# Performance work log

Hardware: AMD Instinct MI355X
Metric: run time of the kernel (lower is better)

Reference implementation:

```python
import jax, jax.numpy as jnp
import numpy as np

B, S, D, H = 2, 2048, 1024, 16
HD = D // H
MAX_SEQ_LEN = 2048
ROPE_BASE = 10000.0


def _rope(x, pos):
    # x: [B,S,H,HD], pos: [B,S] int positions (already abs+clamped)
    inv_freq = 1.0 / (ROPE_BASE ** (jnp.arange(0, HD, 2, dtype=jnp.float32) / HD))  # [HD/2]
    freqs = pos.astype(jnp.float32)[..., None] * inv_freq  # [B,S,HD/2]
    cos = jnp.cos(freqs)[:, :, None, :]  # [B,S,1,HD/2]
    sin = jnp.sin(freqs)[:, :, None, :]
    x1, x2 = x[..., : HD // 2], x[..., HD // 2 :]
    return jnp.concatenate([x1 * cos - x2 * sin, x2 * cos + x1 * sin], axis=-1)


def setup_inputs() -> dict:
    key = jax.random.key(0)
    ks = jax.random.split(key, 8)
    std = 1.0 / np.sqrt(D)
    x = jax.random.normal(ks[0], (B, S, D), dtype=jnp.float32)
    Wq = jax.random.normal(ks[1], (D, D), dtype=jnp.float32) * std
    Wk = jax.random.normal(ks[2], (D, D), dtype=jnp.float32) * std
    Wv = jax.random.normal(ks[3], (D, D), dtype=jnp.float32) * std
    Wo = jax.random.normal(ks[4], (D, D), dtype=jnp.float32) * std
    bq = jnp.zeros((D,), jnp.float32)
    bk = jnp.zeros((D,), jnp.float32)
    bv = jnp.zeros((D,), jnp.float32)
    bo = jnp.zeros((D,), jnp.float32)
    decay_rate = jnp.float32(0.1)
    # causal mask [B,S,S]
    mask = jnp.broadcast_to(jnp.tril(jnp.ones((S, S), jnp.int32)), (B, S, S))
    # sorted day offsets per batch (monotone time axis)
    days_offset = jnp.sort(jax.random.randint(ks[5], (B, S), 0, MAX_SEQ_LEN), axis=-1).astype(jnp.int32)
    return {"x": x, "Wq": Wq, "bq": bq, "Wk": Wk, "bk": bk, "Wv": Wv, "bv": bv,
            "Wo": Wo, "bo": bo, "decay_rate": decay_rate, "mask": mask, "days_offset": days_offset}


def reference(x, Wq, bq, Wk, bk, Wv, bv, Wo, bo, decay_rate, mask, days_offset):
    b, s, _ = x.shape
    q = (x @ Wq.T + bq).reshape(b, s, H, HD)
    k = (x @ Wk.T + bk).reshape(b, s, H, HD)
    v = (x @ Wv.T + bv).reshape(b, s, H, HD)
    pos = jnp.clip(jnp.abs(days_offset), 0, MAX_SEQ_LEN - 1)
    q = _rope(q, pos)
    k = _rope(k, pos)
    scores = jnp.einsum("bqhd,bkhd->bhqk", q, k) / np.sqrt(HD).astype(np.float32)
    dist = jnp.abs(days_offset[:, :, None] - days_offset[:, None, :]).astype(jnp.float32)  # [B,S,S]
    decay = jnp.exp(-decay_rate * dist)
    scores = scores * decay[:, None, :, :]
    scores = jnp.where(mask[:, None, :, :] == 0, -jnp.inf, scores)
    attn = jax.nn.softmax(scores, axis=-1)
    out = jnp.einsum("bhqk,bkhd->bqhd", attn, v).reshape(b, s, D)
    return out @ Wo.T + bo
```

## Files before the change

### kernel.cpp

```cpp
#include <hip/hip_runtime.h>
#include <hip/hip_bf16.h>


typedef unsigned short u16;
typedef short bf16x8 __attribute__((ext_vector_type(8)));
typedef float f32x4 __attribute__((ext_vector_type(4)));

__device__ __forceinline__ u16 f2bf(float f) {
    unsigned u = __builtin_bit_cast(unsigned, f);
    u += 0x7fffu + ((u >> 16) & 1u);
    return (u16)(u >> 16);
}
__device__ __forceinline__ float bf2f(u16 h) {
    unsigned u = ((unsigned)h) << 16;
    return __builtin_bit_cast(float, u);
}

__global__ __launch_bounds__(256) void convert_all_k(const float* __restrict__ x,
                                                     const float* __restrict__ wq,
                                                     const float* __restrict__ wk,
                                                     const float* __restrict__ wv,
                                                     const float* __restrict__ wo_,
                                                     u16* __restrict__ xb,
                                                     u16* __restrict__ wqkv,
                                                     u16* __restrict__ wob) {
    int i = (blockIdx.x * 256 + threadIdx.x) * 4;
    const float* src;
    u16* dst;
    int off;
    if (i < 4194304) {
        src = x; dst = xb; off = i;
    } else if (i < 5242880) {
        src = wq; dst = wqkv; off = i - 4194304;
    } else if (i < 6291456) {
        src = wk; dst = wqkv + 1048576; off = i - 5242880;
    } else if (i < 7340032) {
        src = wv; dst = wqkv + 2097152; off = i - 6291456;
    } else {
        src = wo_; dst = wob; off = i - 7340032;
    }
    float4 v = *(const float4*)(src + off);
    uint2 o;
    o.x = (unsigned)f2bf(v.x) | ((unsigned)f2bf(v.y) << 16);
    o.y = (unsigned)f2bf(v.z) | ((unsigned)f2bf(v.w) << 16);
    *(uint2*)(dst + off) = o;
}

template <int EPI>
__global__ __launch_bounds__(256) void gemm_bt(const u16* __restrict__ A,
                                               const u16* __restrict__ Bw,
                                               const float* __restrict__ bias0,
                                               const float* __restrict__ bias1,
                                               const float* __restrict__ bias2,
                                               const int* __restrict__ days,
                                               u16* __restrict__ outB,
                                               float* __restrict__ outF,
                                               int M, int N, int K) {
    __shared__ __align__(16) u16 As[2][4096];
    __shared__ __align__(16) u16 Bs[2][4096];
    const int tid = threadIdx.x;
    const int lane = tid & 63;
    const int w = tid >> 6;
    const int wr = w >> 1, wc = w & 1;
    const int lr = lane & 15, lg = lane >> 4;
    const int nbn = N >> 7;
    const int m0 = (blockIdx.x / nbn) << 7;
    const int n0 = (blockIdx.x % nbn) << 7;

    f32x4 acc[4][4] = {};

    const u16* aptr[2];
    const u16* bptr[2];
    int ldsoff[2];
#pragma unroll
    for (int i = 0; i < 2; ++i) {
        int c = (w * 2 + i) * 64 + lane;
        int row = c >> 2, kc = (c & 3) << 3;
        aptr[i] = A + (size_t)(m0 + row) * K + kc;
        bptr[i] = Bw + (size_t)(n0 + row) * K + kc;
        ldsoff[i] = (w * 2 + i) * 512;
    }

#define GSTAGE(K0, BUF)                                                                \
    do {                                                                               \
        _Pragma("unroll") for (int i = 0; i < 2; ++i) {                                \
            __builtin_amdgcn_global_load_lds(                                          \
                (const __attribute__((address_space(1))) void*)(aptr[i] + (K0)),       \
                (__attribute__((address_space(3))) void*)(&As[BUF][ldsoff[i]]), 16, 0, \
                0);                                                                    \
            __builtin_amdgcn_global_load_lds(                                          \
                (const __attribute__((address_space(1))) void*)(bptr[i] + (K0)),       \
                (__attribute__((address_space(3))) void*)(&Bs[BUF][ldsoff[i]]), 16, 0, \
                0);                                                                    \
        }                                                                              \
    } while (0)

    const int nks = K >> 5;
    GSTAGE(0, 0);
    for (int ks = 0; ks < nks; ++ks) {
        const int cur = ks & 1;
        if (ks + 1 < nks) {
            GSTAGE((ks + 1) * 32, cur ^ 1);
            asm volatile("s_waitcnt vmcnt(4)" ::: "memory");
        } else {
            asm volatile("s_waitcnt vmcnt(0)" ::: "memory");
        }
        __builtin_amdgcn_s_barrier();
        bf16x8 af[4], bfr[4];
#pragma unroll
        for (int i = 0; i < 4; ++i)
            af[i] = *(const bf16x8*)(&As[cur][(wr * 64 + i * 16 + lr) * 32 + lg * 8]);
#pragma unroll
        for (int j = 0; j < 4; ++j)
            bfr[j] = *(const bf16x8*)(&Bs[cur][(wc * 64 + j * 16 + lr) * 32 + lg * 8]);
#pragma unroll
        for (int i = 0; i < 4; ++i)
#pragma unroll
            for (int j = 0; j < 4; ++j)
                acc[i][j] = __builtin_amdgcn_mfma_f32_16x16x32_bf16(af[i], bfr[j],
                                                                    acc[i][j], 0, 0, 0);
        __builtin_amdgcn_s_barrier();
    }
#undef GSTAGE

    auto bsel = [&](int ng) -> float {
        if (EPI != 0) return bias0[ng];
        return (ng < 1024) ? bias0[ng] : (ng < 2048) ? bias1[ng - 1024] : bias2[ng - 2048];
    };

    if (EPI == 0 && (n0 + wc * 64) < 2048) {
        const float C1 = -0.41524101186091903f;
        const float inv0 = exp2f((float)lr * C1);
        const float inv1 = exp2f((float)(16 + lr) * C1);
#pragma unroll
        for (int i = 0; i < 4; ++i) {
            int mg = m0 + wr * 64 + i * 16 + lg * 4;
#pragma unroll
            for (int r = 0; r < 4; ++r) {
                int m = mg + r;
                int d = days[m];
                int ad = d < 0 ? -d : d;
                ad = ad > 2047 ? 2047 : ad;
                float pos = (float)ad;
#pragma unroll
                for (int j = 0; j < 2; ++j) {
                    int ng1 = n0 + wc * 64 + j * 16 + lr;
                    int ng2 = ng1 + 32;
                    float x1 = acc[i][j][r] + bsel(ng1);
                    float x2 = acc[i][j + 2][r] + bsel(ng2);
                    float ang = pos * (j ? inv1 : inv0);
                    float sn, cs;
                    __sincosf(ang, &sn, &cs);
                    outB[(size_t)m * N + ng1] = f2bf(x1 * cs - x2 * sn);
                    outB[(size_t)m * N + ng2] = f2bf(x2 * cs + x1 * sn);
                }
            }
        }
    } else {
#pragma unroll
        for (int i = 0; i < 4; ++i) {
            int mg = m0 + wr * 64 + i * 16 + lg * 4;
#pragma unroll
            for (int j = 0; j < 4; ++j) {
                int ng = n0 + wc * 64 + j * 16 + lr;
                float bias = bsel(ng);
#pragma unroll
                for (int r = 0; r < 4; ++r) {
                    float v = acc[i][j][r] + bias;
                    if (EPI == 0)
                        outB[(size_t)(mg + r) * N + ng] = f2bf(v);
                    else
                        outF[(size_t)(mg + r) * N + ng] = v;
                }
            }
        }
    }
}

__global__ __launch_bounds__(256) void v_transpose_k(const u16* __restrict__ qkv,
                                                     u16* __restrict__ vt) {
    __shared__ u16 tile[64][66];
    int st = blockIdx.x & 31;
    int bh = blockIdx.x >> 5;
    int b = bh >> 4, h = bh & 15;
    int s0 = st * 64;
    int t = threadIdx.x;
#pragma unroll
    for (int it = 0; it < 16; ++it) {
        int idx = it * 256 + t;
        int sr = idx >> 6, c = idx & 63;
        tile[sr][c] = qkv[(size_t)(b * 2048 + s0 + sr) * 3072 + 2048 + h * 64 + c];
    }
    __syncthreads();
#pragma unroll
    for (int it = 0; it < 16; ++it) {
        int idx = it * 256 + t;
        int hd = idx >> 6, sc = idx & 63;
        vt[((size_t)(bh * 64 + hd)) * 2048 + s0 + sc] = tile[sc][hd];
    }
}

__device__ __forceinline__ void attn_tile(const u16* __restrict__ Ks,
                                          const u16* __restrict__ Vs,
                                          u16* __restrict__ Pw,
                                          const int* __restrict__ dbk,
                                          float dkmax_c, bf16x8 pconst, float pcr,
                                          bf16x8 bq0, bf16x8 bq1, float dq_c, float c1,
                                          int qrel, bool domask,
                                          float& l_part, f32x4* acc, int lr, int lg) {
    if (!domask && __all(dkmax_c - dq_c < -20.0f)) {
        l_part += 16.0f * pcr;
        __builtin_amdgcn_s_setprio(1);
#pragma unroll
        for (int pv = 0; pv < 2; ++pv) {
            int chunk = pv * 4 + lg;
#pragma unroll
            for (int c = 0; c < 4; ++c) {
                const int r3 = c * 16 + lr;
                bf16x8 bv = *(const bf16x8*)(Vs + r3 * 64 + ((chunk ^ (r3 & 7)) << 3));
                acc[c] = __builtin_amdgcn_mfma_f32_16x16x32_bf16(pconst, bv, acc[c], 0, 0, 0);
            }
        }
        __builtin_amdgcn_s_setprio(0);
        return;
    }
    f32x4 st_acc[4];
    __builtin_amdgcn_s_setprio(1);
#pragma unroll
    for (int st = 0; st < 4; ++st) {
        const int r2 = st * 16 + lr;
        const u16* kr = Ks + r2 * 64;
        bf16x8 ka0 = *(const bf16x8*)(kr + ((lg ^ (r2 & 7)) << 3));
        bf16x8 ka1 = *(const bf16x8*)(kr + (((4 + lg) ^ (r2 & 7)) << 3));
        f32x4 t = {};
        t = __builtin_amdgcn_mfma_f32_16x16x32_bf16(ka0, bq0, t, 0, 0, 0);
        t = __builtin_amdgcn_mfma_f32_16x16x32_bf16(ka1, bq1, t, 0, 0, 0);
        st_acc[st] = t;
    }
    __builtin_amdgcn_s_setprio(0);
    const float L2E = 1.4426950408889634f;
    const float POFF = 17.312340490667562f;
    float p[4][4];
#pragma unroll
    for (int st = 0; st < 4; ++st) {
        int4 dk4 = *(const int4*)(dbk + st * 16 + lg * 4);
#pragma unroll
        for (int r = 0; r < 4; ++r) {
            float dkf = (float)((&dk4.x)[r]);
            float dec = exp2f(__builtin_fmaf(dkf, c1, -dq_c));
            float v = st_acc[st][r] * dec;
            p[st][r] = exp2f(__builtin_fmaf(v, L2E, -POFF));
        }
    }
    if (domask) {
#pragma unroll
        for (int st = 0; st < 4; ++st)
#pragma unroll
            for (int r = 0; r < 4; ++r)
                p[st][r] = (st * 16 + lg * 4 + r <= qrel) ? p[st][r] : 0.f;
    }
#pragma unroll
    for (int st = 0; st < 4; ++st)
#pragma unroll
        for (int r = 0; r < 4; ++r) l_part += p[st][r];
#pragma unroll
    for (int st = 0; st < 4; ++st) {
        unsigned lo, hi;
        asm("v_cvt_pk_bf16_f32 %0, %1, %2" : "=v"(lo) : "v"(p[st][0]), "v"(p[st][1]));
        asm("v_cvt_pk_bf16_f32 %0, %1, %2" : "=v"(hi) : "v"(p[st][2]), "v"(p[st][3]));
        uint2 pk;
        pk.x = lo;
        pk.y = hi;
        int chunk = st * 2 + (lg >> 1);
        int idx = lr * 64 + ((chunk ^ (lr & 7)) << 3) + ((lg & 1) << 2);
        *(uint2*)&Pw[idx] = pk;
    }
    __builtin_amdgcn_s_setprio(1);
#pragma unroll
    for (int pv = 0; pv < 2; ++pv) {
        int chunk = pv * 4 + lg;
        bf16x8 pa = *(const bf16x8*)&Pw[lr * 64 + ((chunk ^ (lr & 7)) << 3)];
#pragma unroll
        for (int c = 0; c < 4; ++c) {
            const int r3 = c * 16 + lr;
            bf16x8 bv = *(const bf16x8*)(Vs + r3 * 64 + ((chunk ^ (r3 & 7)) << 3));
            acc[c] = __builtin_amdgcn_mfma_f32_16x16x32_bf16(pa, bv, acc[c], 0, 0, 0);
        }
    }
    __builtin_amdgcn_s_setprio(0);
}

__global__ __launch_bounds__(512, 4) void attn_k(const u16* __restrict__ qkv,
                                                 const u16* __restrict__ vt,
                                                 const int* __restrict__ days,
                                                 const float* __restrict__ decay_p,
                                                 u16* __restrict__ attn_out) {
    __shared__ __align__(16) u16 Ks[4][4096];
    __shared__ __align__(16) u16 Vs[4][4096];
    __shared__ __align__(16) u16 Plds[8][1024];
    const int tid = threadIdx.x;
    const int lane = tid & 63;
    const int w = tid >> 6;
    const int qw = w & 3;
    const int g = w >> 2;
    const int lr = lane & 15, lg = lane >> 4;
    const int wg = (blockIdx.x & 7) * 64 + (blockIdx.x >> 3);
    const int j = wg & 15;
    const int bh = wg >> 4;
    const int b = bh >> 4, h = bh & 15;
    const int qtB = 31 - j;
    const int qbA = j * 64 + qw * 16;
    const int qbB = qtB * 64 + qw * 16;
    const float rate = decay_p[0];
    const float c1 = rate * 1.4426950408889634f;

    const u16* qmat = qkv + (size_t)b * 2048 * 3072 + h * 64;
    const u16* kmat = qmat + 1024;
    const u16* vtm = vt + (size_t)bh * 64 * 2048;
    const int* db = days + b * 2048;

    const int cp0 = (qw * 2 + 0) * 64 + lane;
    const int cp1 = (qw * 2 + 1) * 64 + lane;
    const int r0 = cp0 >> 3, c0 = cp0 & 7;
    const int r1 = cp1 >> 3, c1i = cp1 & 7;
    const u16* ksrc0 = kmat + (size_t)r0 * 3072 + ((c0 ^ (r0 & 7)) << 3);
    const u16* ksrc1 = kmat + (size_t)r1 * 3072 + ((c1i ^ (r1 & 7)) << 3);
    const u16* vsrc0 = vtm + (size_t)r0 * 2048 + ((c0 ^ (r0 & 7)) << 3);
    const u16* vsrc1 = vtm + (size_t)r1 * 2048 + ((c1i ^ (r1 & 7)) << 3);
    const int doff0 = (qw * 2 + 0) * 512;
    const int doff1 = (qw * 2 + 1) * 512;

#define STAGE(T, SLOT)                                                                 \
    do {                                                                               \
        __builtin_amdgcn_global_load_lds(                                              \
            (const __attribute__((address_space(1))) void*)(ksrc0 +                    \
                                                            (size_t)(T) * 64 * 3072), \
            (__attribute__((address_space(3))) void*)(&Ks[SLOT][doff0]), 16, 0, 0);    \
        __builtin_amdgcn_global_load_lds(                                              \
            (const __attribute__((address_space(1))) void*)(ksrc1 +                    \
                                                            (size_t)(T) * 64 * 3072), \
            (__attribute__((address_space(3))) void*)(&Ks[SLOT][doff1]), 16, 0, 0);    \
        __builtin_amdgcn_global_load_lds(                                              \
            (const __attribute__((address_space(1))) void*)(vsrc0 + (size_t)(T) * 64), \
            (__attribute__((address_space(3))) void*)(&Vs[SLOT][doff0]), 16, 0, 0);    \
        __builtin_amdgcn_global_load_lds(                                              \
            (const __attribute__((address_space(1))) void*)(vsrc1 + (size_t)(T) * 64), \
            (__attribute__((address_space(3))) void*)(&Vs[SLOT][doff1]), 16, 0, 0);    \
    } while (0)

    STAGE(g, g);

    bf16x8 bqA0, bqA1, bqB0, bqB1;
    {
        const u16* qpA = qmat + (size_t)(qbA + lr) * 3072 + lg * 8;
        bqA0 = *(const bf16x8*)qpA;
        bqA1 = *(const bf16x8*)(qpA + 32);
        const u16* qpB = qmat + (size_t)(qbB + lr) * 3072 + lg * 8;
        bqB0 = *(const bf16x8*)qpB;
        bqB1 = *(const bf16x8*)(qpB + 32);
    }
    const float dq_cA = (float)db[qbA + lr] * c1 + 3.0f;
    const float dq_cB = (float)db[qbB + lr] * c1 + 3.0f;

    const u16 pcu = f2bf(exp2f(-17.312340490667562f));
    const float pcr = bf2f(pcu);
    bf16x8 pconst;
#pragma unroll
    for (int i = 0; i < 8; ++i) pconst[i] = (short)pcu;

    float lA = 0.f, lB = 0.f;
    f32x4 accA[4] = {};
    f32x4 accB[4] = {};

    const int nkt = (33 - j) >> 1;
    for (int it = 0; it < nkt; ++it) {
        const int kt = 2 * it + g;
        const int cur = ((it & 1) << 1) + g;
        if (it + 1 < nkt) {
            STAGE(2 * (it + 1) + g, (((it + 1) & 1) << 1) + g);
            asm volatile("s_waitcnt vmcnt(4)" ::: "memory");
        } else {
            asm volatile("s_waitcnt vmcnt(0)" ::: "memory");
        }
        __builtin_amdgcn_s_barrier();
        const int* dbk = db + kt * 64;
        const float dkmax_c = (float)dbk[63] * c1;
        if (kt <= qtB)
            attn_tile(Ks[cur], Vs[cur], Plds[w], dbk, dkmax_c, pconst, pcr,
                      bqB0, bqB1, dq_cB, c1, qw * 16 + lr, kt == qtB, lB, accB, lr, lg);
        if (kt <= j)
            attn_tile(Ks[cur], Vs[cur], Plds[w], dbk, dkmax_c, pconst, pcr,
                      bqA0, bqA1, dq_cA, c1, qw * 16 + lr, kt == j, lA, accA, lr, lg);
        __builtin_amdgcn_s_barrier();
    }
#undef STAGE

    float* xch = (float*)&Plds[0][0];
    float* lx = (float*)&Ks[0][0];
#pragma unroll
    for (int t = 0; t < 2; ++t) {
        float lp = t ? lA : lB;
        f32x4* acc = t ? accA : accB;
        const int qt = t ? j : qtB;
        __syncthreads();
        if (g == 1) {
            float* dst = xch + qw * 1024 + lane * 16;
#pragma unroll
            for (int c = 0; c < 4; ++c) *(f32x4*)(dst + c * 4) = acc[c];
            lx[qw * 64 + lane] = lp;
        }
        __syncthreads();
        if (g == 0) {
            const float* src = xch + qw * 1024 + lane * 16;
#pragma unroll
            for (int c = 0; c < 4; ++c) acc[c] += *(const f32x4*)(src + c * 4);
            lp += lx[qw * 64 + lane];
            float l_full = lp + __shfl_xor(lp, 16);
            l_full += __shfl_xor(l_full, 32);
            float inv_[4];
#pragma unroll
            for (int r = 0; r < 4; ++r) inv_[r] = 1.0f / __shfl(l_full, lg * 4 + r);
#pragma unroll
            for (int c = 0; c < 4; ++c)
#pragma unroll
                for (int r = 0; r < 4; ++r) {
                    const int qg = qt * 64 + qw * 16 + lg * 4 + r;
                    attn_out[(size_t)(b * 2048 + qg) * 1024 + h * 64 + c * 16 + lr] =
                        f2bf(acc[c][r] * inv_[r]);
                }
        }
    }
}

extern "C" void kernel_launch(void* const* d_in, const int* in_sizes, int n_in,
                              void* d_out, int out_size, void* d_ws, size_t ws_size,
                              hipStream_t stream) {
    const float* x = (const float*)d_in[0];
    const float* Wq = (const float*)d_in[1];
    const float* bq = (const float*)d_in[2];
    const float* Wk = (const float*)d_in[3];
    const float* bk = (const float*)d_in[4];
    const float* Wv = (const float*)d_in[5];
    const float* bv = (const float*)d_in[6];
    const float* Wo = (const float*)d_in[7];
    const float* bo = (const float*)d_in[8];
    const float* decay = (const float*)d_in[9];
    const int* days = (const int*)d_in[11];
    float* out = (float*)d_out;

    char* ws = (char*)d_ws;
    u16* xb = (u16*)(ws);
    u16* wqkv = (u16*)(ws + 8388608);
    u16* wo = (u16*)(ws + 14680064);
    u16* qkvb = (u16*)(ws + 16777216);
    u16* vtb = (u16*)(ws + 41943040);
    u16* attb = (u16*)(ws + 50331648);

    convert_all_k<<<8192, 256, 0, stream>>>(x, Wq, Wk, Wv, Wo, xb, wqkv, wo);

    gemm_bt<0><<<768, 256, 0, stream>>>(xb, wqkv, bq, bk, bv, days, qkvb, nullptr,
                                        4096, 3072, 1024);
    v_transpose_k<<<1024, 256, 0, stream>>>(qkvb, vtb);
    attn_k<<<512, 512, 0, stream>>>(qkvb, vtb, days, decay, attb);
    gemm_bt<1><<<256, 256, 0, stream>>>(attb, wo, bo, nullptr, nullptr, days, nullptr,
                                        out, 4096, 1024, 1024);
}
```

Measured before the change: 111.5 us.

## Skip fully-decayed key tiles using precomputed V prefix sums in attention

Adds a small kernel that computes per-tile prefix sums of V for each batch-head. The attention kernel then finds the leading run of key tiles whose decay forces every probability to the constant floor value, and seeds the accumulator and normaliser from the prefix sums instead of iterating over those tiles. The attention kernel is also restructured from paired query tiles split across two wave groups into one query tile per 256-thread block, which removes the cross-group LDS reduction. The cost is an extra launch and a workspace buffer, plus less even work across blocks because causal query tiles are no longer paired.

```diff
diff --git a/kernel.cpp b/kernel.cpp
--- a/kernel.cpp
+++ b/kernel.cpp
@@ -200,6 +200,37 @@
     }
 }
 
+__global__ __launch_bounds__(256) void vps_k(const u16* __restrict__ vt,
+                                             float* __restrict__ vps) {
+    __shared__ float ts[32][32];
+    const int bh = blockIdx.x >> 1;
+    const int d0 = (blockIdx.x & 1) * 32;
+    const int dl = threadIdx.x >> 3;
+    const int seg = threadIdx.x & 7;
+    const u16* vrow = vt + ((size_t)bh * 64 + d0 + dl) * 2048 + seg * 256;
+#pragma unroll
+    for (int tt = 0; tt < 4; ++tt) {
+        float s = 0.f;
+#pragma unroll
+        for (int i = 0; i < 8; ++i) {
+            bf16x8 v = *(const bf16x8*)(vrow + tt * 64 + i * 8);
+#pragma unroll
+            for (int e = 0; e < 8; ++e) s += bf2f((u16)v[e]);
+        }
+        ts[dl][seg * 4 + tt] = s;
+    }
+    __syncthreads();
+    if (threadIdx.x < 32) {
+        int d = threadIdx.x;
+        float acc = 0.f;
+        for (int t = 0; t <= 32; ++t) {
+            vps[((size_t)bh * 33 + t) * 64 + d0 + d] = acc;
+            if (t < 32) acc += ts[d][t];
+        }
+    }
+}
+
+
 __device__ __forceinline__ void attn_tile(const u16* __restrict__ Ks,
                                           const u16* __restrict__ Vs,
                                           u16* __restrict__ Pw,
@@ -290,27 +321,24 @@
     __builtin_amdgcn_s_setprio(0);
 }
 
-__global__ __launch_bounds__(512, 4) void attn_k(const u16* __restrict__ qkv,
+__global__ __launch_bounds__(256, 4) void attn_k(const u16* __restrict__ qkv,
                                                  const u16* __restrict__ vt,
                                                  const int* __restrict__ days,
                                                  const float* __restrict__ decay_p,
+                                                 const float* __restrict__ vps,
                                                  u16* __restrict__ attn_out) {
-    __shared__ __align__(16) u16 Ks[4][4096];
-    __shared__ __align__(16) u16 Vs[4][4096];
-    __shared__ __align__(16) u16 Plds[8][1024];
+    __shared__ __align__(16) u16 Ks[2][4096];
+    __shared__ __align__(16) u16 Vs[2][4096];
+    __shared__ __align__(16) u16 Plds[4][1024];
     const int tid = threadIdx.x;
     const int lane = tid & 63;
     const int w = tid >> 6;
-    const int qw = w & 3;
-    const int g = w >> 2;
     const int lr = lane & 15, lg = lane >> 4;
-    const int wg = (blockIdx.x & 7) * 64 + (blockIdx.x >> 3);
-    const int j = wg & 15;
-    const int bh = wg >> 4;
+    const int wg = (blockIdx.x & 7) * 128 + (blockIdx.x >> 3);
+    const int qt = wg & 31;
+    const int bh = wg >> 5;
     const int b = bh >> 4, h = bh & 15;
-    const int qtB = 31 - j;
-    const int qbA = j * 64 + qw * 16;
-    const int qbB = qtB * 64 + qw * 16;
+    const int qb = qt * 64 + w * 16;
     const float rate = decay_p[0];
     const float c1 = rate * 1.4426950408889634f;
 
@@ -319,16 +347,16 @@
     const u16* vtm = vt + (size_t)bh * 64 * 2048;
     const int* db = days + b * 2048;
 
-    const int cp0 = (qw * 2 + 0) * 64 + lane;
-    const int cp1 = (qw * 2 + 1) * 64 + lane;
+    const int cp0 = (w * 2 + 0) * 64 + lane;
+    const int cp1 = (w * 2 + 1) * 64 + lane;
     const int r0 = cp0 >> 3, c0 = cp0 & 7;
     const int r1 = cp1 >> 3, c1i = cp1 & 7;
     const u16* ksrc0 = kmat + (size_t)r0 * 3072 + ((c0 ^ (r0 & 7)) << 3);
     const u16* ksrc1 = kmat + (size_t)r1 * 3072 + ((c1i ^ (r1 & 7)) << 3);
     const u16* vsrc0 = vtm + (size_t)r0 * 2048 + ((c0 ^ (r0 & 7)) << 3);
     const u16* vsrc1 = vtm + (size_t)r1 * 2048 + ((c1i ^ (r1 & 7)) << 3);
-    const int doff0 = (qw * 2 + 0) * 512;
-    const int doff1 = (qw * 2 + 1) * 512;
+    const int doff0 = (w * 2 + 0) * 512;
+    const int doff1 = (w * 2 + 1) * 512;
 
 #define STAGE(T, SLOT)                                                                 \
     do {                                                                               \
@@ -348,19 +376,25 @@
             (__attribute__((address_space(3))) void*)(&Vs[SLOT][doff1]), 16, 0, 0);    \
     } while (0)
 
-    STAGE(g, g);
-
-    bf16x8 bqA0, bqA1, bqB0, bqB1;
+    const float dq00_c = (float)db[qt * 64] * c1 + 3.0f;
+    int t0;
     {
-        const u16* qpA = qmat + (size_t)(qbA + lr) * 3072 + lg * 8;
-        bqA0 = *(const bf16x8*)qpA;
-        bqA1 = *(const bf16x8*)(qpA + 32);
-        const u16* qpB = qmat + (size_t)(qbB + lr) * 3072 + lg * 8;
-        bqB0 = *(const bf16x8*)qpB;
-        bqB1 = *(const bf16x8*)(qpB + 32);
-    }
-    const float dq_cA = (float)db[qbA + lr] * c1 + 3.0f;
-    const float dq_cB = (float)db[qbB + lr] * c1 + 3.0f;
+        const int l32 = lane & 31;
+        float dm = (float)db[l32 * 64 + 63] * c1;
+        bool cnd = (lane < qt) && (dm < dq00_c - 20.0f);
+        unsigned long long m = __ballot(cnd);
+        t0 = (int)__builtin_ctzll(~m);
+    }
+
+    STAGE(t0, 0);
+
+    bf16x8 bq0, bq1;
+    {
+        const u16* qp = qmat + (size_t)(qb + lr) * 3072 + lg * 8;
+        bq0 = *(const bf16x8*)qp;
+        bq1 = *(const bf16x8*)(qp + 32);
+    }
+    const float dq_c = (float)db[qb + lr] * c1 + 3.0f;
 
     const u16 pcu = f2bf(exp2f(-17.312340490667562f));
     const float pcr = bf2f(pcu);
@@ -368,16 +402,18 @@
 #pragma unroll
     for (int i = 0; i < 8; ++i) pconst[i] = (short)pcu;
 
-    float lA = 0.f, lB = 0.f;
-    f32x4 accA[4] = {};
-    f32x4 accB[4] = {};
-
-    const int nkt = (33 - j) >> 1;
-    for (int it = 0; it < nkt; ++it) {
-        const int kt = 2 * it + g;
-        const int cur = ((it & 1) << 1) + g;
-        if (it + 1 < nkt) {
-            STAGE(2 * (it + 1) + g, (((it + 1) & 1) << 1) + g);
+    float lp = (float)t0 * 16.0f * pcr;
+    f32x4 acc[4];
+#pragma unroll
+    for (int c = 0; c < 4; ++c) {
+        float vv = pcr * vps[((size_t)bh * 33 + t0) * 64 + c * 16 + lr];
+        acc[c] = (f32x4){vv, vv, vv, vv};
+    }
+
+    for (int kt = t0; kt <= qt; ++kt) {
+        const int cur = (kt - t0) & 1;
+        if (kt < qt) {
+            STAGE(kt + 1, cur ^ 1);
             asm volatile("s_waitcnt vmcnt(4)" ::: "memory");
         } else {
             asm volatile("s_waitcnt vmcnt(0)" ::: "memory");
@@ -385,51 +421,25 @@
         __builtin_amdgcn_s_barrier();
         const int* dbk = db + kt * 64;
         const float dkmax_c = (float)dbk[63] * c1;
-        if (kt <= qtB)
-            attn_tile(Ks[cur], Vs[cur], Plds[w], dbk, dkmax_c, pconst, pcr,
-                      bqB0, bqB1, dq_cB, c1, qw * 16 + lr, kt == qtB, lB, accB, lr, lg);
-        if (kt <= j)
-            attn_tile(Ks[cur], Vs[cur], Plds[w], dbk, dkmax_c, pconst, pcr,
-                      bqA0, bqA1, dq_cA, c1, qw * 16 + lr, kt == j, lA, accA, lr, lg);
+        attn_tile(Ks[cur], Vs[cur], Plds[w], dbk, dkmax_c, pconst, pcr,
+                  bq0, bq1, dq_c, c1, w * 16 + lr, kt == qt, lp, acc, lr, lg);
         __builtin_amdgcn_s_barrier();
     }
 #undef STAGE
 
-    float* xch = (float*)&Plds[0][0];
-    float* lx = (float*)&Ks[0][0];
-#pragma unroll
-    for (int t = 0; t < 2; ++t) {
-        float lp = t ? lA : lB;
-        f32x4* acc = t ? accA : accB;
-        const int qt = t ? j : qtB;
-        __syncthreads();
-        if (g == 1) {
-            float* dst = xch + qw * 1024 + lane * 16;
-#pragma unroll
-            for (int c = 0; c < 4; ++c) *(f32x4*)(dst + c * 4) = acc[c];
-            lx[qw * 64 + lane] = lp;
-        }
-        __syncthreads();
-        if (g == 0) {
-            const float* src = xch + qw * 1024 + lane * 16;
-#pragma unroll
-            for (int c = 0; c < 4; ++c) acc[c] += *(const f32x4*)(src + c * 4);
-            lp += lx[qw * 64 + lane];
-            float l_full = lp + __shfl_xor(lp, 16);
-            l_full += __shfl_xor(l_full, 32);
-            float inv_[4];
-#pragma unroll
-            for (int r = 0; r < 4; ++r) inv_[r] = 1.0f / __shfl(l_full, lg * 4 + r);
-#pragma unroll
-            for (int c = 0; c < 4; ++c)
-#pragma unroll
-                for (int r = 0; r < 4; ++r) {
-                    const int qg = qt * 64 + qw * 16 + lg * 4 + r;
-                    attn_out[(size_t)(b * 2048 + qg) * 1024 + h * 64 + c * 16 + lr] =
-                        f2bf(acc[c][r] * inv_[r]);
-                }
-        }
-    }
+    float l_full = lp + __shfl_xor(lp, 16);
+    l_full += __shfl_xor(l_full, 32);
+    float inv_[4];
+#pragma unroll
+    for (int r = 0; r < 4; ++r) inv_[r] = 1.0f / __shfl(l_full, lg * 4 + r);
+#pragma unroll
+    for (int c = 0; c < 4; ++c)
+#pragma unroll
+        for (int r = 0; r < 4; ++r) {
+            const int qg = qb + lg * 4 + r;
+            attn_out[(size_t)(b * 2048 + qg) * 1024 + h * 64 + c * 16 + lr] =
+                f2bf(acc[c][r] * inv_[r]);
+        }
 }
 
 extern "C" void kernel_launch(void* const* d_in, const int* in_sizes, int n_in,
@@ -455,13 +465,15 @@
     u16* qkvb = (u16*)(ws + 16777216);
     u16* vtb = (u16*)(ws + 41943040);
     u16* attb = (u16*)(ws + 50331648);
+    float* vpsb = (float*)(ws + 58720256);
 
     convert_all_k<<<8192, 256, 0, stream>>>(x, Wq, Wk, Wv, Wo, xb, wqkv, wo);
 
     gemm_bt<0><<<768, 256, 0, stream>>>(xb, wqkv, bq, bk, bv, days, qkvb, nullptr,
                                         4096, 3072, 1024);
     v_transpose_k<<<1024, 256, 0, stream>>>(qkvb, vtb);
-    attn_k<<<512, 512, 0, stream>>>(qkvb, vtb, days, decay, attb);
+    vps_k<<<64, 256, 0, stream>>>(vtb, vpsb);
+    attn_k<<<1024, 256, 0, stream>>>(qkvb, vtb, days, decay, vpsb, attb);
     gemm_bt<1><<<256, 256, 0, stream>>>(attb, wo, bo, nullptr, nullptr, days, nullptr,
                                         out, 4096, 1024, 1024);
 }
```

New measurement: 105.3 us. 5.6% less time.
